# Kernel tuning notes

Hardware: AMD Instinct MI355X
Metric: run time of the kernel (lower is better)

## Reference

```python
import jax, jax.numpy as jnp
import numpy as np
from jax import lax

INP = 512
OUT = 512
T = 2048
B = 64


def setup_inputs() -> dict:
    key = jax.random.key(0)
    ks = jax.random.split(key, 7)
    rang = (1.0 / OUT) ** 0.5
    u = lambda k, shape: jax.random.uniform(k, shape, jnp.float32, -rang, rang)
    return {
        "x": jax.random.normal(ks[0], (T, B, INP), jnp.float32),
        "g": u(ks[1], (INP, OUT)),
        "gb": u(ks[2], (OUT,)),
        "h": u(ks[3], (INP, OUT)),
        "hb": u(ks[4], (OUT,)),
        "r": u(ks[5], (1, OUT)),
        "rb": u(ks[6], (OUT,)),
    }


def reference(x, g, gb, h, hb, r, rb):
    # x: [T, B, inp]
    Tn = x.shape[0]
    # time gate: r_t = 2*sigmoid((n/T) * r + rb), shape [T, out]
    t = (jnp.arange(Tn, dtype=x.dtype) / Tn)[:, None]  # [T, 1]
    rt = 2.0 * jax.nn.sigmoid(t * r[0] + rb)           # [T, out]
    # precompute per-step gates (vectorized over T)
    G = jax.nn.sigmoid(jnp.einsum("tbi,io->tbo", x, g) + gb) * rt[:, None, :]
    H = jnp.tanh(jnp.einsum("tbi,io->tbo", x, h) + hb) * rt[:, None, :]

    def step(y, gh):
        g_t, h_t = gh
        return y * g_t + h_t, None

    y0 = jnp.zeros((x.shape[1], x.shape[2] * 0 + G.shape[-1]), dtype=x.dtype)
    y, _ = lax.scan(step, y0, (G, H))
    return y
```

## Files before the change

kernel.cpp:

```cpp
#include <hip/hip_runtime.h>
#include <cstdint>
#include <cstddef>

#define TT   2048
#define BB   64
#define KK   512
#define OO   512
#define OT   64
#define NCH  128
#define TC   16
#define LJ   8

typedef __attribute__((ext_vector_type(8))) short short8;
typedef __attribute__((ext_vector_type(4))) float f32x4;

__device__ __forceinline__ unsigned short f2bf(float f) {
  unsigned int u = __float_as_uint(f);
  unsigned int rounding = 0x7FFFu + ((u >> 16) & 1u);
  return (unsigned short)((u + rounding) >> 16);
}

__device__ __forceinline__ float sigmoid_f(float z) {
  return 1.0f / (1.0f + __expf(-z));
}

__device__ __forceinline__ float tanh_f(float z) {
  z = fminf(15.0f, fmaxf(-15.0f, z));
  float e = __expf(-2.0f * z);
  return (1.0f - e) / (1.0f + e);
}

__device__ __forceinline__ void async_ld16(const void* g, void* l) {
  __builtin_amdgcn_global_load_lds(
      (const __attribute__((address_space(1))) void*)g,
      (__attribute__((address_space(3))) void*)l, 16, 0, 0);
}

__global__ void convert_x_k(const float4* __restrict__ x4,
                            ushort4* __restrict__ xb4, int n4) {
  int i = blockIdx.x * blockDim.x + threadIdx.x;
  int stride = gridDim.x * blockDim.x;
  for (; i < n4; i += stride) {
    float4 v = x4[i];
    ushort4 o;
    o.x = f2bf(v.x); o.y = f2bf(v.y); o.z = f2bf(v.z); o.w = f2bf(v.w);
    xb4[i] = o;
  }
}

__global__ void prep_weights_k(const float* __restrict__ g,
                               const float* __restrict__ h,
                               unsigned short* __restrict__ Gt,
                               unsigned short* __restrict__ Ht) {
  __shared__ float tile[32][33];
  const float* src = (blockIdx.z == 0) ? g : h;
  unsigned short* dst = (blockIdx.z == 0) ? Gt : Ht;
  int ox = blockIdx.x * 32;
  int ky = blockIdx.y * 32;
  int tx = threadIdx.x, ty = threadIdx.y;
  #pragma unroll
  for (int r = ty; r < 32; r += 8)
    tile[r][tx] = src[(ky + r) * OO + ox + tx];
  __syncthreads();
  #pragma unroll
  for (int r = ty; r < 32; r += 8)
    dst[(size_t)(ox + r) * KK + ky + tx] = f2bf(tile[tx][r]);
}

__global__ __launch_bounds__(256, 2) void rnn_fused_k(
    const unsigned short* __restrict__ xb,
    const unsigned short* __restrict__ Gt,
    const unsigned short* __restrict__ Ht,
    const float* __restrict__ gb, const float* __restrict__ hb,
    const float* __restrict__ r,  const float* __restrict__ rb,
    float* __restrict__ chunkA, float* __restrict__ chunkB) {
  __shared__ __align__(16) unsigned short Atile[128 * 64];
  __shared__ __align__(16) unsigned short Btile[128 * 64];

  const int tid  = threadIdx.x;
  const int wave = tid >> 6;
  const int lane = tid & 63;
  const int quad = lane >> 4;
  const int lcol = lane & 15;
  const int ot = blockIdx.x & 7;
  const int c  = blockIdx.x >> 3;
  const int o0 = ot * OT;
  const int o  = o0 + wave * 16 + lcol;

  const float gbv = gb[o], hbv = hb[o];
  const float rv  = r[o],  rbv = rb[o];

  float SA[16], SB[16];
  #pragma unroll
  for (int s = 0; s < 16; s++) { SA[s] = 1.0f; SB[s] = 0.0f; }

  const int srow = lane >> 3;
  const int schunk = lane & 7;

  for (int j = 0; j < LJ; j++) {
    const int t0 = c * TC + j * 2;
    const long R0 = (long)t0 * BB;

    f32x4 acc[8][2];
    #pragma unroll
    for (int m = 0; m < 8; m++) {
      f32x4 z = {0.0f, 0.0f, 0.0f, 0.0f};
      acc[m][0] = z; acc[m][1] = z;
    }

    for (int kc = 0; kc < 8; kc++) {
      __syncthreads();
      #pragma unroll
      for (int i = 0; i < 4; i++) {
        int row = wave * 32 + i * 8 + srow;
        int gchunk = schunk ^ (row & 7);
        const unsigned short* gp =
            xb + (R0 + row) * (long)KK + kc * 64 + gchunk * 8;
        async_ld16(gp, &Atile[(wave * 32 + i * 8) * 64]);
      }
      #pragma unroll
      for (int i = 0; i < 4; i++) {
        int row = wave * 32 + i * 8 + srow;
        int gchunk = schunk ^ (row & 7);
        const unsigned short* Wb = (wave < 2) ? Gt : Ht;
        int wrow = o0 + (row & 63);
        const unsigned short* gp =
            Wb + (size_t)wrow * KK + kc * 64 + gchunk * 8;
        async_ld16(gp, &Btile[(wave * 32 + i * 8) * 64]);
      }
      __syncthreads();

      #pragma unroll
      for (int ks = 0; ks < 2; ks++) {
        int lchunk = ks * 4 + quad;
        int bgrow = wave * 16 + lcol;
        short8 bg = *(const short8*)&Btile[bgrow * 64 + ((lchunk ^ (bgrow & 7)) * 8)];
        int bhrow = 64 + wave * 16 + lcol;
        short8 bh = *(const short8*)&Btile[bhrow * 64 + ((lchunk ^ (bhrow & 7)) * 8)];
        #pragma unroll
        for (int m = 0; m < 8; m++) {
          int arow = m * 16 + lcol;
          short8 a = *(const short8*)&Atile[arow * 64 + ((lchunk ^ (arow & 7)) * 8)];
          acc[m][0] = __builtin_amdgcn_mfma_f32_16x16x32_bf16(a, bg, acc[m][0], 0, 0, 0);
          acc[m][1] = __builtin_amdgcn_mfma_f32_16x16x32_bf16(a, bh, acc[m][1], 0, 0, 0);
        }
      }
    }

    const float rt0 = 2.0f * sigmoid_f(((float)t0       * (1.0f / TT)) * rv + rbv);
    const float rt1 = 2.0f * sigmoid_f(((float)(t0 + 1) * (1.0f / TT)) * rv + rbv);
    #pragma unroll
    for (int mq = 0; mq < 4; mq++) {
      #pragma unroll
      for (int reg = 0; reg < 4; reg++) {
        float G0 = sigmoid_f(acc[mq][0][reg] + gbv) * rt0;
        float H0 = tanh_f  (acc[mq][1][reg] + hbv) * rt0;
        float G1 = sigmoid_f(acc[mq + 4][0][reg] + gbv) * rt1;
        float H1 = tanh_f  (acc[mq + 4][1][reg] + hbv) * rt1;
        float pA = G1 * G0;
        float pB = fmaf(G1, H0, H1);
        int s = mq * 4 + reg;
        SB[s] = fmaf(pA, SB[s], pB);
        SA[s] *= pA;
      }
    }
  }

  #pragma unroll
  for (int s = 0; s < 16; s++) {
    int b = (s >> 2) * 16 + quad * 4 + (s & 3);
    size_t idx = ((size_t)c * BB + b) * OO + o;
    chunkA[idx] = SA[s];
    chunkB[idx] = SB[s];
  }
}

__global__ void combine_k(const float* __restrict__ cA,
                          const float* __restrict__ cB,
                          float* __restrict__ out) {
  int i = blockIdx.x * blockDim.x + threadIdx.x;
  float y = 0.0f;
  for (int c = 0; c < NCH; c++) {
    float A  = cA[(size_t)c * (BB * OO) + i];
    float Bv = cB[(size_t)c * (BB * OO) + i];
    y = fmaf(A, y, Bv);
  }
  out[i] = y;
}

extern "C" void kernel_launch(void* const* d_in, const int* in_sizes, int n_in,
                              void* d_out, int out_size, void* d_ws, size_t ws_size,
                              hipStream_t stream) {
  (void)in_sizes; (void)n_in; (void)out_size; (void)ws_size;
  const float* x  = (const float*)d_in[0];
  const float* g  = (const float*)d_in[1];
  const float* gb = (const float*)d_in[2];
  const float* h  = (const float*)d_in[3];
  const float* hb = (const float*)d_in[4];
  const float* r  = (const float*)d_in[5];
  const float* rb = (const float*)d_in[6];
  float* out = (float*)d_out;

  char* w = (char*)d_ws;
  unsigned short* xb = (unsigned short*)w;
  unsigned short* Gt = (unsigned short*)(w + 134217728);
  unsigned short* Ht = (unsigned short*)(w + 134742016);
  float* chunkA = (float*)(w + 135266304);
  float* chunkB = (float*)(w + 152043520);

  const int n4 = (TT * BB * KK) / 4;
  convert_x_k<<<8192, 256, 0, stream>>>((const float4*)x, (ushort4*)xb, n4);
  prep_weights_k<<<dim3(16, 16, 2), dim3(32, 8), 0, stream>>>(g, h, Gt, Ht);
  rnn_fused_k<<<NCH * (OO / OT), 256, 0, stream>>>(xb, Gt, Ht, gb, hb, r, rb,
                                                   chunkA, chunkB);
  combine_k<<<(BB * OO) / 256, 256, 0, stream>>>(chunkA, chunkB, out);
}
```

Baseline: 609.3 us.

## Keep weight slice resident in LDS and double-buffer x tiles over longer chunks

Reduces time chunks from 128 to 32, so each block processes 64 timesteps and loads its full 128x512 bf16 G/H weight slice into LDS once instead of restaging it every k-chunk. x tiles are double-buffered with async loads so the next tile loads while MFMAs run, and waves are rearranged into a 2x2 tiling over batch and output columns. The x conversion kernel is widened to pack 8 bf16 per store, and the combine kernel is unrolled. This trades occupancy (one 256-thread block per CU with 160KB LDS, 256 blocks total) for weight reuse and overlap.

New measurement: 713.1 us. 1.17x slower.

```diff
diff --git a/kernel.cpp b/kernel.cpp
--- a/kernel.cpp
+++ b/kernel.cpp
@@ -7,17 +7,17 @@
 #define KK   512
 #define OO   512
 #define OT   64
-#define NCH  128
-#define TC   16
-#define LJ   8
+#define NCH  32
+#define TC   64
+#define NIT  256
 
 typedef __attribute__((ext_vector_type(8))) short short8;
 typedef __attribute__((ext_vector_type(4))) float f32x4;
 
-__device__ __forceinline__ unsigned short f2bf(float f) {
+__device__ __forceinline__ unsigned int f2bf(float f) {
   unsigned int u = __float_as_uint(f);
   unsigned int rounding = 0x7FFFu + ((u >> 16) & 1u);
-  return (unsigned short)((u + rounding) >> 16);
+  return (u + rounding) >> 16;
 }
 
 __device__ __forceinline__ float sigmoid_f(float z) {
@@ -37,14 +37,18 @@
 }
 
 __global__ void convert_x_k(const float4* __restrict__ x4,
-                            ushort4* __restrict__ xb4, int n4) {
+                            uint4* __restrict__ xb8, int n8) {
   int i = blockIdx.x * blockDim.x + threadIdx.x;
   int stride = gridDim.x * blockDim.x;
-  for (; i < n4; i += stride) {
-    float4 v = x4[i];
-    ushort4 o;
-    o.x = f2bf(v.x); o.y = f2bf(v.y); o.z = f2bf(v.z); o.w = f2bf(v.w);
-    xb4[i] = o;
+  for (; i < n8; i += stride) {
+    float4 a = x4[2 * i];
+    float4 b = x4[2 * i + 1];
+    uint4 o;
+    o.x = f2bf(a.x) | (f2bf(a.y) << 16);
+    o.y = f2bf(a.z) | (f2bf(a.w) << 16);
+    o.z = f2bf(b.x) | (f2bf(b.y) << 16);
+    o.w = f2bf(b.z) | (f2bf(b.w) << 16);
+    xb8[i] = o;
   }
 }
 
@@ -64,115 +68,158 @@
   __syncthreads();
   #pragma unroll
   for (int r = ty; r < 32; r += 8)
-    dst[(size_t)(ox + r) * KK + ky + tx] = f2bf(tile[tx][r]);
-}
-
-__global__ __launch_bounds__(256, 2) void rnn_fused_k(
+    dst[(size_t)(ox + r) * KK + ky + tx] = (unsigned short)f2bf(tile[tx][r]);
+}
+
+__global__ __launch_bounds__(256, 1) void rnn_fused2_k(
     const unsigned short* __restrict__ xb,
     const unsigned short* __restrict__ Gt,
     const unsigned short* __restrict__ Ht,
     const float* __restrict__ gb, const float* __restrict__ hb,
     const float* __restrict__ r,  const float* __restrict__ rb,
     float* __restrict__ chunkA, float* __restrict__ chunkB) {
-  __shared__ __align__(16) unsigned short Atile[128 * 64];
-  __shared__ __align__(16) unsigned short Btile[128 * 64];
+  extern __shared__ __align__(16) unsigned short smem[];
+  unsigned short* Wlds = smem;
+  unsigned short* Ab   = smem + 65536;
 
   const int tid  = threadIdx.x;
   const int wave = tid >> 6;
   const int lane = tid & 63;
   const int quad = lane >> 4;
   const int lcol = lane & 15;
-  const int ot = blockIdx.x & 7;
-  const int c  = blockIdx.x >> 3;
+  const int srow8 = lane >> 3;
+  const int sch   = lane & 7;
+
+  const int bi = blockIdx.x;
+  const int q  = bi >> 3;
+  const int c  = (bi & 7) * 4 + (q >> 3);
+  const int ot = q & 7;
   const int o0 = ot * OT;
-  const int o  = o0 + wave * 16 + lcol;
-
-  const float gbv = gb[o], hbv = hb[o];
-  const float rv  = r[o],  rbv = rb[o];
+
+  const int ow = wave & 1;
+  const int bh = wave >> 1;
+  const int ob = o0 + ow * 32;
+
+  float gbv[2], hbv[2], rv[2], rbv[2];
+  #pragma unroll
+  for (int n = 0; n < 2; n++) {
+    int o = ob + n * 16 + lcol;
+    gbv[n] = gb[o]; hbv[n] = hb[o]; rv[n] = r[o]; rbv[n] = rb[o];
+  }
+
+  for (int rr = 0; rr < 32; ++rr) {
+    int row = wave * 32 + rr;
+    const unsigned short* Wsrc = (row < 64)
+        ? (Gt + (size_t)(o0 + row) * KK)
+        : (Ht + (size_t)(o0 + row - 64) * KK);
+    int gch = (lane & 56) | ((lane & 7) ^ (row & 7));
+    async_ld16(Wsrc + gch * 8, Wlds + row * 512);
+  }
+
+  auto stage_a = [&](int n, int pbuf) {
+    int jj = n >> 3, kcc = n & 7;
+    size_t R0 = (size_t)(c * TC + jj * 2) * BB;
+    unsigned short* dst = Ab + pbuf * 8192;
+    #pragma unroll
+    for (int ii = 0; ii < 4; ++ii) {
+      int row = wave * 32 + ii * 8 + srow8;
+      int gch = sch ^ (row & 7);
+      const unsigned short* gp = xb + (R0 + row) * KK + kcc * 64 + gch * 8;
+      async_ld16(gp, dst + (wave * 32 + ii * 8) * 64);
+    }
+  };
+
+  stage_a(0, 0);
+  __syncthreads();
 
   float SA[16], SB[16];
   #pragma unroll
   for (int s = 0; s < 16; s++) { SA[s] = 1.0f; SB[s] = 0.0f; }
 
-  const int srow = lane >> 3;
-  const int schunk = lane & 7;
-
-  for (int j = 0; j < LJ; j++) {
-    const int t0 = c * TC + j * 2;
-    const long R0 = (long)t0 * BB;
-
-    f32x4 acc[8][2];
-    #pragma unroll
-    for (int m = 0; m < 8; m++) {
+  f32x4 acc[4][4];
+  #pragma unroll
+  for (int a = 0; a < 4; a++)
+    #pragma unroll
+    for (int b = 0; b < 4; b++) {
       f32x4 z = {0.0f, 0.0f, 0.0f, 0.0f};
-      acc[m][0] = z; acc[m][1] = z;
-    }
-
-    for (int kc = 0; kc < 8; kc++) {
-      __syncthreads();
-      #pragma unroll
-      for (int i = 0; i < 4; i++) {
-        int row = wave * 32 + i * 8 + srow;
-        int gchunk = schunk ^ (row & 7);
-        const unsigned short* gp =
-            xb + (R0 + row) * (long)KK + kc * 64 + gchunk * 8;
-        async_ld16(gp, &Atile[(wave * 32 + i * 8) * 64]);
+      acc[a][b] = z;
+    }
+
+  int p = 0;
+  for (int it = 0; it < NIT; ++it) {
+    if (it + 1 < NIT) stage_a(it + 1, p ^ 1);
+
+    const unsigned short* A0 = Ab + p * 8192;
+    const int kc = it & 7;
+    #pragma unroll
+    for (int ks = 0; ks < 2; ++ks) {
+      short8 bfr[4];
+      #pragma unroll
+      for (int n = 0; n < 2; ++n)
+        #pragma unroll
+        for (int gh = 0; gh < 2; ++gh) {
+          int rowb = gh * 64 + ow * 32 + n * 16 + lcol;
+          int cb = kc * 8 + ks * 4 + quad;
+          int slot = (cb & ~7) | ((cb & 7) ^ (rowb & 7));
+          bfr[n * 2 + gh] = *(const short8*)(Wlds + rowb * 512 + slot * 8);
+        }
+      #pragma unroll
+      for (int am = 0; am < 4; ++am) {
+        int arow = (am >> 1) * 64 + bh * 32 + (am & 1) * 16 + lcol;
+        int lc = ks * 4 + quad;
+        int slot = lc ^ (arow & 7);
+        short8 afr = *(const short8*)(A0 + arow * 64 + slot * 8);
+        #pragma unroll
+        for (int bn = 0; bn < 4; ++bn)
+          acc[am][bn] = __builtin_amdgcn_mfma_f32_16x16x32_bf16(
+              afr, bfr[bn], acc[am][bn], 0, 0, 0);
       }
-      #pragma unroll
-      for (int i = 0; i < 4; i++) {
-        int row = wave * 32 + i * 8 + srow;
-        int gchunk = schunk ^ (row & 7);
-        const unsigned short* Wb = (wave < 2) ? Gt : Ht;
-        int wrow = o0 + (row & 63);
-        const unsigned short* gp =
-            Wb + (size_t)wrow * KK + kc * 64 + gchunk * 8;
-        async_ld16(gp, &Btile[(wave * 32 + i * 8) * 64]);
+    }
+
+    if ((it & 7) == 7) {
+      const int j = it >> 3;
+      const int t0 = c * TC + j * 2;
+      #pragma unroll
+      for (int n = 0; n < 2; ++n) {
+        float rt0 = 2.0f * sigmoid_f(((float)t0       * (1.0f / TT)) * rv[n] + rbv[n]);
+        float rt1 = 2.0f * sigmoid_f(((float)(t0 + 1) * (1.0f / TT)) * rv[n] + rbv[n]);
+        #pragma unroll
+        for (int mt = 0; mt < 2; ++mt)
+          #pragma unroll
+          for (int reg = 0; reg < 4; ++reg) {
+            float G0 = sigmoid_f(acc[mt    ][n * 2 + 0][reg] + gbv[n]) * rt0;
+            float H0 = tanh_f  (acc[mt    ][n * 2 + 1][reg] + hbv[n]) * rt0;
+            float G1 = sigmoid_f(acc[2 + mt][n * 2 + 0][reg] + gbv[n]) * rt1;
+            float H1 = tanh_f  (acc[2 + mt][n * 2 + 1][reg] + hbv[n]) * rt1;
+            float pA = G1 * G0;
+            float pB = fmaf(G1, H0, H1);
+            int s = (n * 2 + mt) * 4 + reg;
+            SB[s] = fmaf(pA, SB[s], pB);
+            SA[s] *= pA;
+            acc[mt][n * 2 + 0][reg] = 0.0f;
+            acc[mt][n * 2 + 1][reg] = 0.0f;
+            acc[2 + mt][n * 2 + 0][reg] = 0.0f;
+            acc[2 + mt][n * 2 + 1][reg] = 0.0f;
+          }
       }
-      __syncthreads();
-
-      #pragma unroll
-      for (int ks = 0; ks < 2; ks++) {
-        int lchunk = ks * 4 + quad;
-        int bgrow = wave * 16 + lcol;
-        short8 bg = *(const short8*)&Btile[bgrow * 64 + ((lchunk ^ (bgrow & 7)) * 8)];
-        int bhrow = 64 + wave * 16 + lcol;
-        short8 bh = *(const short8*)&Btile[bhrow * 64 + ((lchunk ^ (bhrow & 7)) * 8)];
-        #pragma unroll
-        for (int m = 0; m < 8; m++) {
-          int arow = m * 16 + lcol;
-          short8 a = *(const short8*)&Atile[arow * 64 + ((lchunk ^ (arow & 7)) * 8)];
-          acc[m][0] = __builtin_amdgcn_mfma_f32_16x16x32_bf16(a, bg, acc[m][0], 0, 0, 0);
-          acc[m][1] = __builtin_amdgcn_mfma_f32_16x16x32_bf16(a, bh, acc[m][1], 0, 0, 0);
-        }
+    }
+    __syncthreads();
+    p ^= 1;
+  }
+
+  #pragma unroll
+  for (int n = 0; n < 2; ++n)
+    #pragma unroll
+    for (int mt = 0; mt < 2; ++mt)
+      #pragma unroll
+      for (int reg = 0; reg < 4; ++reg) {
+        int s = (n * 2 + mt) * 4 + reg;
+        int b = bh * 32 + mt * 16 + quad * 4 + reg;
+        int o = ob + n * 16 + lcol;
+        size_t idx = ((size_t)c * BB + b) * OO + o;
+        chunkA[idx] = SA[s];
+        chunkB[idx] = SB[s];
       }
-    }
-
-    const float rt0 = 2.0f * sigmoid_f(((float)t0       * (1.0f / TT)) * rv + rbv);
-    const float rt1 = 2.0f * sigmoid_f(((float)(t0 + 1) * (1.0f / TT)) * rv + rbv);
-    #pragma unroll
-    for (int mq = 0; mq < 4; mq++) {
-      #pragma unroll
-      for (int reg = 0; reg < 4; reg++) {
-        float G0 = sigmoid_f(acc[mq][0][reg] + gbv) * rt0;
-        float H0 = tanh_f  (acc[mq][1][reg] + hbv) * rt0;
-        float G1 = sigmoid_f(acc[mq + 4][0][reg] + gbv) * rt1;
-        float H1 = tanh_f  (acc[mq + 4][1][reg] + hbv) * rt1;
-        float pA = G1 * G0;
-        float pB = fmaf(G1, H0, H1);
-        int s = mq * 4 + reg;
-        SB[s] = fmaf(pA, SB[s], pB);
-        SA[s] *= pA;
-      }
-    }
-  }
-
-  #pragma unroll
-  for (int s = 0; s < 16; s++) {
-    int b = (s >> 2) * 16 + quad * 4 + (s & 3);
-    size_t idx = ((size_t)c * BB + b) * OO + o;
-    chunkA[idx] = SA[s];
-    chunkB[idx] = SB[s];
-  }
 }
 
 __global__ void combine_k(const float* __restrict__ cA,
@@ -180,6 +227,7 @@
                           float* __restrict__ out) {
   int i = blockIdx.x * blockDim.x + threadIdx.x;
   float y = 0.0f;
+  #pragma unroll
   for (int c = 0; c < NCH; c++) {
     float A  = cA[(size_t)c * (BB * OO) + i];
     float Bv = cB[(size_t)c * (BB * OO) + i];
@@ -206,12 +254,19 @@
   unsigned short* Gt = (unsigned short*)(w + 134217728);
   unsigned short* Ht = (unsigned short*)(w + 134742016);
   float* chunkA = (float*)(w + 135266304);
-  float* chunkB = (float*)(w + 152043520);
-
-  const int n4 = (TT * BB * KK) / 4;
-  convert_x_k<<<8192, 256, 0, stream>>>((const float4*)x, (ushort4*)xb, n4);
+  float* chunkB = (float*)(w + 139460608);
+
+  static bool attr_set = false;
+  if (!attr_set) {
+    hipFuncSetAttribute(reinterpret_cast<const void*>(rnn_fused2_k),
+                        hipFuncAttributeMaxDynamicSharedMemorySize, 163840);
+    attr_set = true;
+  }
+
+  const int n8 = (TT * BB * KK) / 8;
+  convert_x_k<<<4096, 256, 0, stream>>>((const float4*)x, (uint4*)xb, n8);
   prep_weights_k<<<dim3(16, 16, 2), dim3(32, 8), 0, stream>>>(g, h, Gt, Ht);
-  rnn_fused_k<<<NCH * (OO / OT), 256, 0, stream>>>(xb, Gt, Ht, gb, hb, r, rb,
-                                                   chunkA, chunkB);
-  combine_k<<<(BB * OO) / 256, 256, 0, stream>>>(chunkA, chunkB, out);
-}
+  rnn_fused2_k<<<NCH * (OO / OT), 256, 163840, stream>>>(xb, Gt, Ht, gb, hb,
+                                                         r, rb, chunkA, chunkB);
+  combine_k<<<(BB * OO) / 128, 128, 0, stream>>>(chunkA, chunkB, out);
+}
```

## Keep weights in registers and double-buffer full-K x tiles per timestep

Applied to the files above, without the earlier changes.

The fused kernel is restructured so each wave holds its 16 output columns of G and H weights for the full K dimension in registers. Each block stages one whole timestep's x slice (64x512 bf16) into double-buffered LDS with async loads, overlapping the next timestep's load with the current MFMAs. Block shape moves to 512 threads, 128 outputs and 64 chunks of 32 timesteps, which halves the chunk buffers and the combine loop. This removes the per-k-chunk weight reloads and the two syncs per k-chunk, at the cost of 128KB of dynamic LDS, high register use that limits occupancy, and a grid of only 256 blocks.

Measured after the change: 539.5 us. -11.5%, faster.

```diff
diff --git a/kernel.cpp b/kernel.cpp
--- a/kernel.cpp
+++ b/kernel.cpp
@@ -6,10 +6,8 @@
 #define BB   64
 #define KK   512
 #define OO   512
-#define OT   64
-#define NCH  128
-#define TC   16
-#define LJ   8
+#define NCH  64
+#define TC   32
 
 typedef __attribute__((ext_vector_type(8))) short short8;
 typedef __attribute__((ext_vector_type(4))) float f32x4;
@@ -67,112 +65,116 @@
     dst[(size_t)(ox + r) * KK + ky + tx] = f2bf(tile[tx][r]);
 }
 
-__global__ __launch_bounds__(256, 2) void rnn_fused_k(
+__global__ __launch_bounds__(512, 2) void rnn_fused3_k(
     const unsigned short* __restrict__ xb,
     const unsigned short* __restrict__ Gt,
     const unsigned short* __restrict__ Ht,
     const float* __restrict__ gb, const float* __restrict__ hb,
     const float* __restrict__ r,  const float* __restrict__ rb,
     float* __restrict__ chunkA, float* __restrict__ chunkB) {
-  __shared__ __align__(16) unsigned short Atile[128 * 64];
-  __shared__ __align__(16) unsigned short Btile[128 * 64];
+  extern __shared__ __align__(16) unsigned short smem[];
 
   const int tid  = threadIdx.x;
   const int wave = tid >> 6;
   const int lane = tid & 63;
   const int quad = lane >> 4;
   const int lcol = lane & 15;
-  const int ot = blockIdx.x & 7;
-  const int c  = blockIdx.x >> 3;
-  const int o0 = ot * OT;
-  const int o  = o0 + wave * 16 + lcol;
+
+  const int bi = blockIdx.x;
+  const int ot = bi >> 6;
+  const int c  = bi & 63;
+  const int o  = ot * 128 + wave * 16 + lcol;
 
   const float gbv = gb[o], hbv = hb[o];
   const float rv  = r[o],  rbv = rb[o];
 
+  short8 Bg[8][2], Bh[8][2];
+  {
+    const unsigned short* gp = Gt + (size_t)o * KK + quad * 8;
+    const unsigned short* hp = Ht + (size_t)o * KK + quad * 8;
+    #pragma unroll
+    for (int kc = 0; kc < 8; ++kc)
+      #pragma unroll
+      for (int ks = 0; ks < 2; ++ks) {
+        Bg[kc][ks] = *(const short8*)(gp + kc * 64 + ks * 32);
+        Bh[kc][ks] = *(const short8*)(hp + kc * 64 + ks * 32);
+      }
+  }
+
+  auto stage = [&](int trow, int buf) {
+    unsigned short* dst = smem + buf * 32768 + wave * 8 * 512;
+    const unsigned short* src = xb + ((size_t)trow * BB + wave * 8) * KK;
+    #pragma unroll
+    for (int rr = 0; rr < 8; ++rr) {
+      int gch = (lane & ~7) | ((lane & 7) ^ rr);
+      async_ld16(src + rr * KK + gch * 8, dst + rr * 512);
+    }
+  };
+
+  stage(c * TC, 0);
+
   float SA[16], SB[16];
   #pragma unroll
   for (int s = 0; s < 16; s++) { SA[s] = 1.0f; SB[s] = 0.0f; }
 
-  const int srow = lane >> 3;
-  const int schunk = lane & 7;
-
-  for (int j = 0; j < LJ; j++) {
-    const int t0 = c * TC + j * 2;
-    const long R0 = (long)t0 * BB;
-
-    f32x4 acc[8][2];
-    #pragma unroll
-    for (int m = 0; m < 8; m++) {
-      f32x4 z = {0.0f, 0.0f, 0.0f, 0.0f};
-      acc[m][0] = z; acc[m][1] = z;
+  f32x4 accG[4], accH[4];
+  #pragma unroll
+  for (int m = 0; m < 4; m++) {
+    f32x4 z = {0.0f, 0.0f, 0.0f, 0.0f};
+    accG[m] = z; accH[m] = z;
+  }
+
+  __syncthreads();
+
+  int p = 0;
+  for (int it = 0; it < TC; ++it) {
+    if (it + 1 < TC) stage(c * TC + it + 1, p ^ 1);
+
+    const unsigned short* A0 = smem + p * 32768;
+    #pragma unroll
+    for (int kc = 0; kc < 8; ++kc)
+      #pragma unroll
+      for (int ks = 0; ks < 2; ++ks)
+        #pragma unroll
+        for (int mt = 0; mt < 4; ++mt) {
+          int arow = mt * 16 + lcol;
+          int slot = kc * 8 + ((ks * 4 + quad) ^ (arow & 7));
+          short8 a = *(const short8*)(A0 + arow * 512 + slot * 8);
+          accG[mt] = __builtin_amdgcn_mfma_f32_16x16x32_bf16(
+              a, Bg[kc][ks], accG[mt], 0, 0, 0);
+          accH[mt] = __builtin_amdgcn_mfma_f32_16x16x32_bf16(
+              a, Bh[kc][ks], accH[mt], 0, 0, 0);
+        }
+
+    const int t = c * TC + it;
+    const float rt = 2.0f * sigmoid_f(((float)t * (1.0f / TT)) * rv + rbv);
+    #pragma unroll
+    for (int mt = 0; mt < 4; ++mt)
+      #pragma unroll
+      for (int reg = 0; reg < 4; ++reg) {
+        float G = sigmoid_f(accG[mt][reg] + gbv) * rt;
+        float H = tanh_f  (accH[mt][reg] + hbv) * rt;
+        int s = mt * 4 + reg;
+        SB[s] = fmaf(G, SB[s], H);
+        SA[s] *= G;
+        accG[mt][reg] = 0.0f;
+        accH[mt][reg] = 0.0f;
+      }
+
+    __syncthreads();
+    p ^= 1;
+  }
+
+  #pragma unroll
+  for (int mt = 0; mt < 4; ++mt)
+    #pragma unroll
+    for (int reg = 0; reg < 4; ++reg) {
+      int s = mt * 4 + reg;
+      int b = mt * 16 + quad * 4 + reg;
+      size_t idx = ((size_t)c * BB + b) * OO + o;
+      chunkA[idx] = SA[s];
+      chunkB[idx] = SB[s];
     }
-
-    for (int kc = 0; kc < 8; kc++) {
-      __syncthreads();
-      #pragma unroll
-      for (int i = 0; i < 4; i++) {
-        int row = wave * 32 + i * 8 + srow;
-        int gchunk = schunk ^ (row & 7);
-        const unsigned short* gp =
-            xb + (R0 + row) * (long)KK + kc * 64 + gchunk * 8;
-        async_ld16(gp, &Atile[(wave * 32 + i * 8) * 64]);
-      }
-      #pragma unroll
-      for (int i = 0; i < 4; i++) {
-        int row = wave * 32 + i * 8 + srow;
-        int gchunk = schunk ^ (row & 7);
-        const unsigned short* Wb = (wave < 2) ? Gt : Ht;
-        int wrow = o0 + (row & 63);
-        const unsigned short* gp =
-            Wb + (size_t)wrow * KK + kc * 64 + gchunk * 8;
-        async_ld16(gp, &Btile[(wave * 32 + i * 8) * 64]);
-      }
-      __syncthreads();
-
-      #pragma unroll
-      for (int ks = 0; ks < 2; ks++) {
-        int lchunk = ks * 4 + quad;
-        int bgrow = wave * 16 + lcol;
-        short8 bg = *(const short8*)&Btile[bgrow * 64 + ((lchunk ^ (bgrow & 7)) * 8)];
-        int bhrow = 64 + wave * 16 + lcol;
-        short8 bh = *(const short8*)&Btile[bhrow * 64 + ((lchunk ^ (bhrow & 7)) * 8)];
-        #pragma unroll
-        for (int m = 0; m < 8; m++) {
-          int arow = m * 16 + lcol;
-          short8 a = *(const short8*)&Atile[arow * 64 + ((lchunk ^ (arow & 7)) * 8)];
-          acc[m][0] = __builtin_amdgcn_mfma_f32_16x16x32_bf16(a, bg, acc[m][0], 0, 0, 0);
-          acc[m][1] = __builtin_amdgcn_mfma_f32_16x16x32_bf16(a, bh, acc[m][1], 0, 0, 0);
-        }
-      }
-    }
-
-    const float rt0 = 2.0f * sigmoid_f(((float)t0       * (1.0f / TT)) * rv + rbv);
-    const float rt1 = 2.0f * sigmoid_f(((float)(t0 + 1) * (1.0f / TT)) * rv + rbv);
-    #pragma unroll
-    for (int mq = 0; mq < 4; mq++) {
-      #pragma unroll
-      for (int reg = 0; reg < 4; reg++) {
-        float G0 = sigmoid_f(acc[mq][0][reg] + gbv) * rt0;
-        float H0 = tanh_f  (acc[mq][1][reg] + hbv) * rt0;
-        float G1 = sigmoid_f(acc[mq + 4][0][reg] + gbv) * rt1;
-        float H1 = tanh_f  (acc[mq + 4][1][reg] + hbv) * rt1;
-        float pA = G1 * G0;
-        float pB = fmaf(G1, H0, H1);
-        int s = mq * 4 + reg;
-        SB[s] = fmaf(pA, SB[s], pB);
-        SA[s] *= pA;
-      }
-    }
-  }
-
-  #pragma unroll
-  for (int s = 0; s < 16; s++) {
-    int b = (s >> 2) * 16 + quad * 4 + (s & 3);
-    size_t idx = ((size_t)c * BB + b) * OO + o;
-    chunkA[idx] = SA[s];
-    chunkB[idx] = SB[s];
-  }
 }
 
 __global__ void combine_k(const float* __restrict__ cA,
@@ -180,6 +182,7 @@
                           float* __restrict__ out) {
   int i = blockIdx.x * blockDim.x + threadIdx.x;
   float y = 0.0f;
+  #pragma unroll 8
   for (int c = 0; c < NCH; c++) {
     float A  = cA[(size_t)c * (BB * OO) + i];
     float Bv = cB[(size_t)c * (BB * OO) + i];
@@ -206,12 +209,19 @@
   unsigned short* Gt = (unsigned short*)(w + 134217728);
   unsigned short* Ht = (unsigned short*)(w + 134742016);
   float* chunkA = (float*)(w + 135266304);
-  float* chunkB = (float*)(w + 152043520);
+  float* chunkB = (float*)(w + 143654912);
+
+  static bool attr_set = false;
+  if (!attr_set) {
+    hipFuncSetAttribute(reinterpret_cast<const void*>(rnn_fused3_k),
+                        hipFuncAttributeMaxDynamicSharedMemorySize, 131072);
+    attr_set = true;
+  }
 
   const int n4 = (TT * BB * KK) / 4;
   convert_x_k<<<8192, 256, 0, stream>>>((const float4*)x, (ushort4*)xb, n4);
   prep_weights_k<<<dim3(16, 16, 2), dim3(32, 8), 0, stream>>>(g, h, Gt, Ht);
-  rnn_fused_k<<<NCH * (OO / OT), 256, 0, stream>>>(xb, Gt, Ht, gb, hb, r, rb,
-                                                   chunkA, chunkB);
+  rnn_fused3_k<<<NCH * 4, 512, 131072, stream>>>(xb, Gt, Ht, gb, hb, r, rb,
+                                                 chunkA, chunkB);
   combine_k<<<(BB * OO) / 256, 256, 0, stream>>>(chunkA, chunkB, out);
 }
```
